# Optimization experiments

Measured on AMD Instinct MI355X. Metric: run time of the kernel, lower is better.

The kernel has to match this reference:

```python
import jax, jax.numpy as jnp
import numpy as np
import math

GAUSSIAN_KERNEL = 3.0  # sigma from init_kwargs


def setup_inputs() -> dict:
    key = jax.random.key(0)
    k1, k2, k3, k4 = jax.random.split(key, 4)
    B, De, Do, T, H, W = 4, 128, 512, 10, 32, 32
    return {
        "m_in": jax.random.normal(k1, (B, De, T, H, W), dtype=jnp.float32),
        "m_out": jax.random.normal(k2, (B, Do, T, H, W), dtype=jnp.float32),
        "q_in": jax.random.normal(k3, (B, De, H, W), dtype=jnp.float32),
        "q_out": jax.random.normal(k4, (B, Do, H, W), dtype=jnp.float32),
    }


def _gaussian_kernel_map(corr, H, W, sigma):
    # corr: [B, THW, HW]; for each memory location, gaussian centered at its
    # argmax query position over the HxW query grid.
    idx = jnp.argmax(corr, axis=2)                       # [B, THW] int
    idx_y = (idx // W).astype(corr.dtype)[..., None, None]  # [B, THW, 1, 1]
    idx_x = (idx % W).astype(corr.dtype)[..., None, None]
    y = jnp.arange(H, dtype=corr.dtype).reshape(1, 1, H, 1)
    x = jnp.arange(W, dtype=corr.dtype).reshape(1, 1, 1, W)
    g = jnp.exp(-((x - idx_x) ** 2 + (y - idx_y) ** 2) / (2.0 * sigma ** 2))
    return g.reshape(corr.shape)                         # [B, THW, HW]


def reference(m_in, m_out, q_in, q_out):
    B, De, T, H, W = m_in.shape
    Do = m_out.shape[1]
    THW, HW = T * H * W, H * W

    mi = m_in.reshape(B, De, THW)       # [B, De, THW]
    qi = q_in.reshape(B, De, HW)        # [B, De, HW]
    # p[b, t, q] = <memory key t, query key q> / sqrt(De)
    p = jnp.einsum('bdt,bdq->btq', mi, qi) / math.sqrt(De)   # [B, THW, HW]

    gauss = _gaussian_kernel_map(p, H, W, GAUSSIAN_KERNEL)

    # softmax over memory dimension (dim=1), then gaussian reweight + renorm
    p_soft = jax.nn.softmax(p, axis=1)
    p_w = p_soft * gauss
    p_w = p_w / jnp.sum(p_w, axis=1, keepdims=True)

    mo = m_out.reshape(B, Do, THW)
    mem = jnp.einsum('bdt,btq->bdq', mo, p_w).reshape(B, Do, H, W)
    mem_out = jnp.concatenate([mem, q_out], axis=1)      # [B, 2*Do, H, W]
    return mem_out, p_w
```

## Files before the change

kernel.cpp:

```cpp
#include <hip/hip_runtime.h>
#include <hip/hip_bf16.h>

#define BB 4
#define DE 128
#define DO_ 512
#define THW 10240
#define HW 1024
#define SCALE 0.08838834764831845f
#define INV2S2 0.05555555555555555f
#define NCH 32
#define CHT 320

#define WS_PART_F  81920
#define WS_STATS_F 344064
#define WS_MO16_B  1409024ull
#define WS_PWT_B   43352064ull
#define WS_MITH_B  (WS_PWT_B)
#define WS_MITL_B  (WS_PWT_B + 10485760ull)
#define WS_QITH_B  (WS_PWT_B + 20971520ull)
#define WS_QITL_B  (WS_PWT_B + 22020096ull)

using bf16x8 = __attribute__((ext_vector_type(8))) short;
using f16x8  = __attribute__((ext_vector_type(8))) _Float16;
using f32x4  = __attribute__((ext_vector_type(4))) float;
using u16x8  = __attribute__((ext_vector_type(8))) unsigned short;

__device__ __forceinline__ unsigned short f2bf(float f) {
    __hip_bfloat16 h = __float2bfloat16(f);
    return *reinterpret_cast<unsigned short*>(&h);
}
__device__ __forceinline__ void glds16(const void* g, void* l) {
    __builtin_amdgcn_global_load_lds((const __attribute__((address_space(1))) void*)g,
                                     (__attribute__((address_space(3))) void*)l,
                                     16, 0, 0);
}
__device__ __forceinline__ unsigned int ordf(float f) {
    unsigned int u = __float_as_uint(f);
    return (u & 0x80000000u) ? ~u : (u | 0x80000000u);
}

__global__ __launch_bounds__(256) void k_init(float* __restrict__ out,
                                              const float* __restrict__ qout,
                                              float4* __restrict__ amax4)
{
    int idx = blockIdx.x * 256 + threadIdx.x;
    if (idx < 20480) amax4[idx] = make_float4(0.f, 0.f, 0.f, 0.f);
    int b  = idx >> 18;
    int r  = idx & 262143;
    int c  = r >> 8;
    int q4 = r & 255;
    float4* dst = (float4*)out + idx;
    if (c < DO_) {
        *dst = make_float4(0.f, 0.f, 0.f, 0.f);
    } else {
        const float4* src = (const float4*)qout + ((size_t)(b * DO_ + (c - DO_)) << 8) + q4;
        *dst = *src;
    }
}

__global__ __launch_bounds__(256) void k_split(const float* __restrict__ src,
                                               unsigned short* __restrict__ dstH,
                                               unsigned short* __restrict__ dstL,
                                               int ncols, float scale)
{
    __shared__ float tile[128][65];
    int t0 = blockIdx.x * 64;
    int b  = blockIdx.z;
    int tid = threadIdx.x;
    const float* S = src + (size_t)b * DE * ncols + t0;
#pragma unroll
    for (int i = 0; i < 8; ++i) {
        int s  = tid + i * 256;
        int k  = s >> 4;
        int c4 = (s & 15) << 2;
        *(float4*)&tile[k][c4] = *(const float4*)&S[(size_t)k * ncols + c4];
    }
    __syncthreads();
#pragma unroll
    for (int i = 0; i < 4; ++i) {
        int s  = tid + i * 256;
        int t  = s >> 4;
        int k8 = s & 15;
        u16x8 oh, ol;
#pragma unroll
        for (int j = 0; j < 8; ++j) {
            float v = tile[k8 * 8 + j][t] * scale;
            _Float16 h = (_Float16)v;
            float rr = v - (float)h;
            _Float16 l = (_Float16)(rr * 2048.0f);
            oh[j] = *(unsigned short*)&h;
            ol[j] = *(unsigned short*)&l;
        }
        size_t o = ((size_t)b * ncols + t0 + t) * 128 + k8 * 8;
        *(u16x8*)&dstH[o] = oh;
        *(u16x8*)&dstL[o] = ol;
    }
}

__global__ __launch_bounds__(256) void k_gemm1m(const unsigned short* __restrict__ AH,
                                                const unsigned short* __restrict__ AL,
                                                const unsigned short* __restrict__ BH,
                                                const unsigned short* __restrict__ BL,
                                                float* __restrict__ p,
                                                unsigned long long* __restrict__ amax)
{
    __shared__ unsigned short AsH[4096];
    __shared__ unsigned short AsL[4096];
    __shared__ unsigned short BsH[4096];
    __shared__ unsigned short BsL[4096];
    int id  = blockIdx.x;
    int tbg = id & 7;
    int rr  = id >> 3;
    int b   = rr / 80;
    int j   = rr - b * 80;
    int tb  = tbg * 10 + (j >> 3);
    int qb  = j & 7;
    int tid = threadIdx.x;
    int w = tid >> 6, lane = tid & 63;
    int quad = lane >> 4, l15 = lane & 15;

    const char* AgH = (const char*)AH + ((size_t)b * THW + (size_t)tb * 128) * 256;
    const char* AgL = (const char*)AL + ((size_t)b * THW + (size_t)tb * 128) * 256;
    const char* BgH = (const char*)BH + ((size_t)b * HW + qb * 128) * 256;
    const char* BgL = (const char*)BL + ((size_t)b * HW + qb * 128) * 256;

    int srow = lane >> 2;
    int sj   = (lane & 3) ^ (srow & 3);
    size_t ro0 = (size_t)(w * 32 + srow) * 256 + sj * 16;
    size_t ro1 = (size_t)(w * 32 + 16 + srow) * 256 + sj * 16;
    char* lds0[4] = {(char*)AsH + w * 2048, (char*)AsL + w * 2048,
                     (char*)BsH + w * 2048, (char*)BsL + w * 2048};
    const char* gl0[4] = {AgH, AgL, BgH, BgL};

    int wm = w >> 1, wn = w & 1;
    int fq = ((l15 & 3) ^ quad) << 4;
    const char* aFH = (const char*)AsH + (wm * 64 + l15) * 64 + fq;
    const char* aFL = (const char*)AsL + (wm * 64 + l15) * 64 + fq;
    const char* bFH = (const char*)BsH + (wn * 64 + l15) * 64 + fq;
    const char* bFL = (const char*)BsL + (wn * 64 + l15) * 64 + fq;

    f32x4 acc1[4][4], acc2[4][4];
#pragma unroll
    for (int i = 0; i < 4; ++i)
#pragma unroll
        for (int j2 = 0; j2 < 4; ++j2) {
            acc1[i][j2] = (f32x4){0.f, 0.f, 0.f, 0.f};
            acc2[i][j2] = (f32x4){0.f, 0.f, 0.f, 0.f};
        }

    for (int kc = 0; kc < 4; ++kc) {
        size_t kb = (size_t)kc * 64;
        __syncthreads();
#pragma unroll
        for (int m = 0; m < 4; ++m) {
            glds16(gl0[m] + ro0 + kb, lds0[m]);
            glds16(gl0[m] + ro1 + kb, lds0[m] + 1024);
        }
        __syncthreads();
        f16x8 afH[4], afL[4], bfH[4], bfL[4];
#pragma unroll
        for (int i = 0; i < 4; ++i) {
            afH[i] = *(const f16x8*)(aFH + i * 1024);
            afL[i] = *(const f16x8*)(aFL + i * 1024);
            bfH[i] = *(const f16x8*)(bFH + i * 1024);
            bfL[i] = *(const f16x8*)(bFL + i * 1024);
        }
#pragma unroll
        for (int i = 0; i < 4; ++i)
#pragma unroll
            for (int j2 = 0; j2 < 4; ++j2)
                acc1[i][j2] = __builtin_amdgcn_mfma_f32_16x16x32_f16(afH[i], bfH[j2], acc1[i][j2], 0, 0, 0);
#pragma unroll
        for (int i = 0; i < 4; ++i)
#pragma unroll
            for (int j2 = 0; j2 < 4; ++j2)
                acc2[i][j2] = __builtin_amdgcn_mfma_f32_16x16x32_f16(afH[i], bfL[j2], acc2[i][j2], 0, 0, 0);
#pragma unroll
        for (int i = 0; i < 4; ++i)
#pragma unroll
            for (int j2 = 0; j2 < 4; ++j2)
                acc2[i][j2] = __builtin_amdgcn_mfma_f32_16x16x32_f16(afL[i], bfH[j2], acc2[i][j2], 0, 0, 0);
    }

    const float inv2048 = 4.8828125e-4f;
    int t0 = tb * 128 + wm * 64;
    float* Pg = p + ((size_t)b * THW + t0) * HW + qb * 128 + wn * 64;
    int qbase = qb * 128 + wn * 64;
#pragma unroll
    for (int i = 0; i < 4; ++i) {
#pragma unroll
        for (int r = 0; r < 4; ++r) {
            int tl = i * 16 + quad * 4 + r;
            float v[4];
#pragma unroll
            for (int j2 = 0; j2 < 4; ++j2) {
                v[j2] = acc1[i][j2][r] + acc2[i][j2][r] * inv2048;
                Pg[(size_t)tl * HW + j2 * 16 + l15] = v[j2];
            }
            float best = v[0]; int bj = 0;
#pragma unroll
            for (int j2 = 1; j2 < 4; ++j2)
                if (v[j2] > best) { best = v[j2]; bj = j2; }
            int q = qbase + bj * 16 + l15;
            unsigned long long pk = ((unsigned long long)ordf(best) << 32)
                                  | (unsigned long long)(0xFFFFFFFFu - (unsigned)q);
#pragma unroll
            for (int off = 1; off < 16; off <<= 1) {
                unsigned long long o = __shfl_xor(pk, off);
                if (o > pk) pk = o;
            }
            if (l15 == 0)
                atomicMax(&amax[(size_t)b * THW + t0 + tl], pk);
        }
    }
}

__global__ __launch_bounds__(256) void k_colstats(const float* __restrict__ p,
                                                  const unsigned long long* __restrict__ amax,
                                                  float* __restrict__ part)
{
    int q  = blockIdx.x * 256 + threadIdx.x;
    int ch = blockIdx.y, b = blockIdx.z;
    float x = (float)(q & 31), y = (float)(q >> 5);
    const float* pp = p + ((size_t)b * THW + ch * CHT) * HW + q;
    const unsigned long long* am = amax + (size_t)b * THW + ch * CHT;
    float m = -3.0e38f, s = 0.f;
    for (int i = 0; i < CHT; ++i) {
        unsigned idx = 0xFFFFFFFFu - (unsigned)am[i];
        float dx = x - (float)(idx & 31), dy = y - (float)(idx >> 5);
        float z = pp[(size_t)i * HW] - (dx * dx + dy * dy) * INV2S2;
        float nm = fmaxf(m, z);
        s = s * __expf(m - nm) + __expf(z - nm);
        m = nm;
    }
    size_t o = ((size_t)(b * NCH + ch) * HW + q) * 2;
    part[o] = m; part[o + 1] = s;
}

__global__ __launch_bounds__(256) void k_reduce(const float* __restrict__ part,
                                                float* __restrict__ stats)
{
    int i = blockIdx.x * 256 + threadIdx.x;
    int b = i >> 10, q = i & 1023;
    float M = -3.0e38f;
#pragma unroll
    for (int c = 0; c < NCH; ++c)
        M = fmaxf(M, part[((size_t)(b * NCH + c) * HW + q) * 2]);
    float S = 0.f;
#pragma unroll
    for (int c = 0; c < NCH; ++c) {
        size_t o = ((size_t)(b * NCH + c) * HW + q) * 2;
        S += part[o + 1] * __expf(part[o] - M);
    }
    stats[(size_t)i * 2] = M;
    stats[(size_t)i * 2 + 1] = 1.0f / S;
}

__global__ __launch_bounds__(256) void k_pwt(float* __restrict__ p,
                                             const unsigned long long* __restrict__ amax,
                                             const float* __restrict__ stats,
                                             unsigned short* __restrict__ pwT)
{
    __shared__ float tile[64][65];
    __shared__ float ctr[128];
    __shared__ float st[128];
    int qb = blockIdx.x, tb = blockIdx.y, b = blockIdx.z;
    int tid = threadIdx.x;
    if (tid < 64) {
        unsigned idx = 0xFFFFFFFFu - (unsigned)amax[(size_t)b * THW + tb * 64 + tid];
        ctr[tid * 2]     = (float)(idx & 31);
        ctr[tid * 2 + 1] = (float)(idx >> 5);
    }
    if (tid < 128)
        st[tid] = stats[((size_t)b * HW + qb * 64) * 2 + tid];
    __syncthreads();
    int r0 = tid >> 4;
    int c4 = (tid & 15) << 2;
#pragma unroll
    for (int i = 0; i < 4; ++i) {
        int r = r0 + i * 16;
        float* pp = p + ((size_t)b * THW + tb * 64 + r) * HW + qb * 64 + c4;
        float4 v = *(float4*)pp;
        float cx = ctr[r * 2], cy = ctr[r * 2 + 1];
        float vv[4] = {v.x, v.y, v.z, v.w};
#pragma unroll
        for (int j = 0; j < 4; ++j) {
            int q = qb * 64 + c4 + j;
            float x = (float)(q & 31), y = (float)(q >> 5);
            float dx = x - cx, dy = y - cy;
            vv[j] = __expf(vv[j] - (dx * dx + dy * dy) * INV2S2 - st[(c4 + j) * 2])
                    * st[(c4 + j) * 2 + 1];
            tile[r][c4 + j] = vv[j];
        }
        *(float4*)pp = make_float4(vv[0], vv[1], vv[2], vv[3]);
    }
    __syncthreads();
    int ql = tid >> 3;
    int t0 = (tid & 7) << 3;
#pragma unroll
    for (int pass = 0; pass < 2; ++pass) {
        int q = ql + pass * 32;
        u16x8 o8;
#pragma unroll
        for (int j = 0; j < 8; ++j)
            o8[j] = f2bf(tile[t0 + j][q]);
        *(u16x8*)&pwT[((size_t)b * HW + qb * 64 + q) * THW + tb * 64 + t0] = o8;
    }
}

__global__ __launch_bounds__(256) void k_mo16(const float* __restrict__ mo,
                                              unsigned short* __restrict__ o)
{
    size_t base = ((size_t)blockIdx.x * 256 + threadIdx.x) * 8;
    float4 a = *(const float4*)(mo + base);
    float4 c = *(const float4*)(mo + base + 4);
    u16x8 v;
    v[0] = f2bf(a.x); v[1] = f2bf(a.y); v[2] = f2bf(a.z); v[3] = f2bf(a.w);
    v[4] = f2bf(c.x); v[5] = f2bf(c.y); v[6] = f2bf(c.z); v[7] = f2bf(c.w);
    *(u16x8*)(o + base) = v;
}

__global__ __launch_bounds__(256) void k_gemm2m(const unsigned short* __restrict__ A16,
                                                const unsigned short* __restrict__ B16,
                                                float* __restrict__ out)
{
    __shared__ unsigned short As[4096];
    __shared__ unsigned short Bs[4096];
    int id   = blockIdx.x;
    int xcd  = id & 7;
    int rest = id >> 3;
    int shi  = rest >> 5;
    int jj   = rest & 31;
    int s    = xcd + (shi << 3);
    int b    = s >> 2, ks = s & 3;
    int mb   = jj >> 3, nb = jj & 7;
    int tid = threadIdx.x;
    int w = tid >> 6, lane = tid & 63;
    int quad = lane >> 4, l15 = lane & 15;

    const char* Ag = (const char*)(A16 + (size_t)b * DO_ * THW + (size_t)mb * 128 * THW + ks * 2560);
    const char* Bg = (const char*)(B16 + (size_t)b * HW * THW + (size_t)nb * 128 * THW + ks * 2560);

    int srow = lane >> 2;
    int sj   = (lane & 3) ^ (srow & 3);
    const char* aP0 = Ag + (size_t)((w * 2 + 0) * 16 + srow) * (THW * 2) + sj * 16;
    const char* aP1 = Ag + (size_t)((w * 2 + 1) * 16 + srow) * (THW * 2) + sj * 16;
    const char* bP0 = Bg + (size_t)((w * 2 + 0) * 16 + srow) * (THW * 2) + sj * 16;
    const char* bP1 = Bg + (size_t)((w * 2 + 1) * 16 + srow) * (THW * 2) + sj * 16;
    char* lA0 = (char*)As + (w * 2 + 0) * 1024;
    char* lA1 = (char*)As + (w * 2 + 1) * 1024;
    char* lB0 = (char*)Bs + (w * 2 + 0) * 1024;
    char* lB1 = (char*)Bs + (w * 2 + 1) * 1024;

    int wm = w >> 1, wn = w & 1;
    int fq = ((l15 & 3) ^ quad) << 4;
    const char* aF = (const char*)As + (wm * 64 + l15) * 64 + fq;
    const char* bF = (const char*)Bs + (wn * 64 + l15) * 64 + fq;

    f32x4 acc[4][4];
#pragma unroll
    for (int i = 0; i < 4; ++i)
#pragma unroll
        for (int j = 0; j < 4; ++j)
            acc[i][j] = (f32x4){0.f, 0.f, 0.f, 0.f};

    for (int kit = 0; kit < 80; ++kit) {
        int kb = kit * 64;
        __syncthreads();
        glds16(aP0 + kb, lA0);
        glds16(aP1 + kb, lA1);
        glds16(bP0 + kb, lB0);
        glds16(bP1 + kb, lB1);
        __syncthreads();
        bf16x8 af[4], bfr[4];
#pragma unroll
        for (int i = 0; i < 4; ++i) af[i]  = *(const bf16x8*)(aF + i * 1024);
#pragma unroll
        for (int j = 0; j < 4; ++j) bfr[j] = *(const bf16x8*)(bF + j * 1024);
#pragma unroll
        for (int i = 0; i < 4; ++i)
#pragma unroll
            for (int j = 0; j < 4; ++j)
                acc[i][j] = __builtin_amdgcn_mfma_f32_16x16x32_bf16(af[i], bfr[j], acc[i][j], 0, 0, 0);
    }

    float* Cg = out + (size_t)b * (2 * DO_ * HW);
    int d0 = mb * 128 + wm * 64 + quad * 4;
    int q0 = nb * 128 + wn * 64 + l15;
#pragma unroll
    for (int i = 0; i < 4; ++i)
#pragma unroll
        for (int j = 0; j < 4; ++j)
#pragma unroll
            for (int r = 0; r < 4; ++r)
                atomicAdd(&Cg[(size_t)(d0 + i * 16 + r) * HW + q0 + j * 16], acc[i][j][r]);
}

extern "C" void kernel_launch(void* const* d_in, const int* in_sizes, int n_in,
                              void* d_out, int out_size, void* d_ws, size_t ws_size,
                              hipStream_t stream)
{
    const float* m_in  = (const float*)d_in[0];
    const float* m_out = (const float*)d_in[1];
    const float* q_in  = (const float*)d_in[2];
    const float* q_out = (const float*)d_in[3];
    float* out = (float*)d_out;
    float* pw  = out + (size_t)BB * 2 * DO_ * HW;
    float* ws  = (float*)d_ws;
    unsigned long long* amax = (unsigned long long*)d_ws;
    float* part    = ws + WS_PART_F;
    float* stats   = ws + WS_STATS_F;
    unsigned short* mo16  = (unsigned short*)((char*)d_ws + WS_MO16_B);
    unsigned short* pwT16 = (unsigned short*)((char*)d_ws + WS_PWT_B);
    unsigned short* miTH  = (unsigned short*)((char*)d_ws + WS_MITH_B);
    unsigned short* miTL  = (unsigned short*)((char*)d_ws + WS_MITL_B);
    unsigned short* qiTH  = (unsigned short*)((char*)d_ws + WS_QITH_B);
    unsigned short* qiTL  = (unsigned short*)((char*)d_ws + WS_QITL_B);

    hipLaunchKernelGGL(k_init,    dim3(4096),        dim3(256), 0, stream, out, q_out, (float4*)d_ws);
    hipLaunchKernelGGL(k_split,   dim3(160, 1, BB),  dim3(256), 0, stream, m_in, miTH, miTL, THW, 1.0f);
    hipLaunchKernelGGL(k_split,   dim3(16, 1, BB),   dim3(256), 0, stream, q_in, qiTH, qiTL, HW, SCALE);
    hipLaunchKernelGGL(k_gemm1m,  dim3(2560),        dim3(256), 0, stream, miTH, miTL, qiTH, qiTL, pw, amax);
    hipLaunchKernelGGL(k_colstats,dim3(4, NCH, BB),  dim3(256), 0, stream, pw, amax, part);
    hipLaunchKernelGGL(k_reduce,  dim3(16),          dim3(256), 0, stream, part, stats);
    hipLaunchKernelGGL(k_mo16,    dim3(10240),       dim3(256), 0, stream, m_out, mo16);
    hipLaunchKernelGGL(k_pwt,     dim3(16, 160, BB), dim3(256), 0, stream, pw, amax, stats, pwT16);
    hipLaunchKernelGGL(k_gemm2m,  dim3(512),         dim3(256), 0, stream, mo16, pwT16, out);
}
```

Measured before the change: 516.8 us.

## Double-buffer LDS staging in both GEMMs and double split-K in gemm2

Both MFMA GEMM kernels now use two LDS buffers, issuing global-to-LDS loads for the next K chunk before computing on the current one, with explicit vmcnt waits and raw barriers replacing the two syncthreads per iteration. The second GEMM also splits K eight ways instead of four, doubling the grid to 1024 blocks with half the K iterations each. The aim is to hide global load latency and raise occupancy and parallelism on the output GEMM. The cost is doubled shared memory per block, which may reduce resident blocks, and twice as many atomic adds into the output.

```diff
diff --git a/kernel.cpp b/kernel.cpp
--- a/kernel.cpp
+++ b/kernel.cpp
@@ -104,10 +104,10 @@
                                                 float* __restrict__ p,
                                                 unsigned long long* __restrict__ amax)
 {
-    __shared__ unsigned short AsH[4096];
-    __shared__ unsigned short AsL[4096];
-    __shared__ unsigned short BsH[4096];
-    __shared__ unsigned short BsL[4096];
+    __shared__ unsigned short AsH[2][4096];
+    __shared__ unsigned short AsL[2][4096];
+    __shared__ unsigned short BsH[2][4096];
+    __shared__ unsigned short BsL[2][4096];
     int id  = blockIdx.x;
     int tbg = id & 7;
     int rr  = id >> 3;
@@ -128,9 +128,18 @@
     int sj   = (lane & 3) ^ (srow & 3);
     size_t ro0 = (size_t)(w * 32 + srow) * 256 + sj * 16;
     size_t ro1 = (size_t)(w * 32 + 16 + srow) * 256 + sj * 16;
-    char* lds0[4] = {(char*)AsH + w * 2048, (char*)AsL + w * 2048,
-                     (char*)BsH + w * 2048, (char*)BsL + w * 2048};
-    const char* gl0[4] = {AgH, AgL, BgH, BgL};
+
+#define G1_STAGE(BUF, KB) do {                                                          \
+    char* _d;                                                                           \
+    _d = (char*)AsH + (BUF) * 8192 + w * 2048;                                          \
+    glds16(AgH + ro0 + (KB), _d); glds16(AgH + ro1 + (KB), _d + 1024);                  \
+    _d = (char*)AsL + (BUF) * 8192 + w * 2048;                                          \
+    glds16(AgL + ro0 + (KB), _d); glds16(AgL + ro1 + (KB), _d + 1024);                  \
+    _d = (char*)BsH + (BUF) * 8192 + w * 2048;                                          \
+    glds16(BgH + ro0 + (KB), _d); glds16(BgH + ro1 + (KB), _d + 1024);                  \
+    _d = (char*)BsL + (BUF) * 8192 + w * 2048;                                          \
+    glds16(BgL + ro0 + (KB), _d); glds16(BgL + ro1 + (KB), _d + 1024);                  \
+  } while (0)
 
     int wm = w >> 1, wn = w & 1;
     int fq = ((l15 & 3) ^ quad) << 4;
@@ -148,22 +157,25 @@
             acc2[i][j2] = (f32x4){0.f, 0.f, 0.f, 0.f};
         }
 
+    G1_STAGE(0, 0);
+    int cur = 0;
     for (int kc = 0; kc < 4; ++kc) {
-        size_t kb = (size_t)kc * 64;
-        __syncthreads();
-#pragma unroll
-        for (int m = 0; m < 4; ++m) {
-            glds16(gl0[m] + ro0 + kb, lds0[m]);
-            glds16(gl0[m] + ro1 + kb, lds0[m] + 1024);
-        }
-        __syncthreads();
+        if (kc < 3) {
+            G1_STAGE(cur ^ 1, (size_t)(kc + 1) * 64);
+            asm volatile("s_waitcnt vmcnt(8)" ::: "memory");
+        } else {
+            asm volatile("s_waitcnt vmcnt(0)" ::: "memory");
+        }
+        __builtin_amdgcn_s_barrier();
+        __builtin_amdgcn_sched_barrier(0);
+        int cb = cur * 8192;
         f16x8 afH[4], afL[4], bfH[4], bfL[4];
 #pragma unroll
         for (int i = 0; i < 4; ++i) {
-            afH[i] = *(const f16x8*)(aFH + i * 1024);
-            afL[i] = *(const f16x8*)(aFL + i * 1024);
-            bfH[i] = *(const f16x8*)(bFH + i * 1024);
-            bfL[i] = *(const f16x8*)(bFL + i * 1024);
+            afH[i] = *(const f16x8*)(aFH + cb + i * 1024);
+            afL[i] = *(const f16x8*)(aFL + cb + i * 1024);
+            bfH[i] = *(const f16x8*)(bFH + cb + i * 1024);
+            bfL[i] = *(const f16x8*)(bFL + cb + i * 1024);
         }
 #pragma unroll
         for (int i = 0; i < 4; ++i)
@@ -180,7 +192,11 @@
 #pragma unroll
             for (int j2 = 0; j2 < 4; ++j2)
                 acc2[i][j2] = __builtin_amdgcn_mfma_f32_16x16x32_f16(afL[i], bfH[j2], acc2[i][j2], 0, 0, 0);
-    }
+        __builtin_amdgcn_sched_barrier(0);
+        __builtin_amdgcn_s_barrier();
+        cur ^= 1;
+    }
+#undef G1_STAGE
 
     const float inv2048 = 4.8828125e-4f;
     int t0 = tb * 128 + wm * 64;
@@ -324,22 +340,22 @@
                                                 const unsigned short* __restrict__ B16,
                                                 float* __restrict__ out)
 {
-    __shared__ unsigned short As[4096];
-    __shared__ unsigned short Bs[4096];
+    __shared__ unsigned short As[2][4096];
+    __shared__ unsigned short Bs[2][4096];
     int id   = blockIdx.x;
     int xcd  = id & 7;
     int rest = id >> 3;
     int shi  = rest >> 5;
     int jj   = rest & 31;
     int s    = xcd + (shi << 3);
-    int b    = s >> 2, ks = s & 3;
+    int b    = s >> 3, ks = s & 7;
     int mb   = jj >> 3, nb = jj & 7;
     int tid = threadIdx.x;
     int w = tid >> 6, lane = tid & 63;
     int quad = lane >> 4, l15 = lane & 15;
 
-    const char* Ag = (const char*)(A16 + (size_t)b * DO_ * THW + (size_t)mb * 128 * THW + ks * 2560);
-    const char* Bg = (const char*)(B16 + (size_t)b * HW * THW + (size_t)nb * 128 * THW + ks * 2560);
+    const char* Ag = (const char*)(A16 + (size_t)b * DO_ * THW + (size_t)mb * 128 * THW + ks * 1280);
+    const char* Bg = (const char*)(B16 + (size_t)b * HW * THW + (size_t)nb * 128 * THW + ks * 1280);
 
     int srow = lane >> 2;
     int sj   = (lane & 3) ^ (srow & 3);
@@ -352,6 +368,13 @@
     char* lB0 = (char*)Bs + (w * 2 + 0) * 1024;
     char* lB1 = (char*)Bs + (w * 2 + 1) * 1024;
 
+#define G2_STAGE(BUF, KB) do {                          \
+    glds16(aP0 + (KB), lA0 + (BUF) * 8192);             \
+    glds16(aP1 + (KB), lA1 + (BUF) * 8192);             \
+    glds16(bP0 + (KB), lB0 + (BUF) * 8192);             \
+    glds16(bP1 + (KB), lB1 + (BUF) * 8192);             \
+  } while (0)
+
     int wm = w >> 1, wn = w & 1;
     int fq = ((l15 & 3) ^ quad) << 4;
     const char* aF = (const char*)As + (wm * 64 + l15) * 64 + fq;
@@ -364,25 +387,33 @@
         for (int j = 0; j < 4; ++j)
             acc[i][j] = (f32x4){0.f, 0.f, 0.f, 0.f};
 
-    for (int kit = 0; kit < 80; ++kit) {
-        int kb = kit * 64;
-        __syncthreads();
-        glds16(aP0 + kb, lA0);
-        glds16(aP1 + kb, lA1);
-        glds16(bP0 + kb, lB0);
-        glds16(bP1 + kb, lB1);
-        __syncthreads();
+    G2_STAGE(0, 0);
+    int cur = 0;
+    for (int kit = 0; kit < 40; ++kit) {
+        if (kit < 39) {
+            G2_STAGE(cur ^ 1, (size_t)(kit + 1) * 64);
+            asm volatile("s_waitcnt vmcnt(4)" ::: "memory");
+        } else {
+            asm volatile("s_waitcnt vmcnt(0)" ::: "memory");
+        }
+        __builtin_amdgcn_s_barrier();
+        __builtin_amdgcn_sched_barrier(0);
+        int cb = cur * 8192;
         bf16x8 af[4], bfr[4];
 #pragma unroll
-        for (int i = 0; i < 4; ++i) af[i]  = *(const bf16x8*)(aF + i * 1024);
-#pragma unroll
-        for (int j = 0; j < 4; ++j) bfr[j] = *(const bf16x8*)(bF + j * 1024);
+        for (int i = 0; i < 4; ++i) af[i]  = *(const bf16x8*)(aF + cb + i * 1024);
+#pragma unroll
+        for (int j = 0; j < 4; ++j) bfr[j] = *(const bf16x8*)(bF + cb + j * 1024);
 #pragma unroll
         for (int i = 0; i < 4; ++i)
 #pragma unroll
             for (int j = 0; j < 4; ++j)
                 acc[i][j] = __builtin_amdgcn_mfma_f32_16x16x32_bf16(af[i], bfr[j], acc[i][j], 0, 0, 0);
-    }
+        __builtin_amdgcn_sched_barrier(0);
+        __builtin_amdgcn_s_barrier();
+        cur ^= 1;
+    }
+#undef G2_STAGE
 
     float* Cg = out + (size_t)b * (2 * DO_ * HW);
     int d0 = mb * 128 + wm * 64 + quad * 4;
@@ -425,5 +456,5 @@
     hipLaunchKernelGGL(k_reduce,  dim3(16),          dim3(256), 0, stream, part, stats);
     hipLaunchKernelGGL(k_mo16,    dim3(10240),       dim3(256), 0, stream, m_out, mo16);
     hipLaunchKernelGGL(k_pwt,     dim3(16, 160, BB), dim3(256), 0, stream, pw, amax, stats, pwT16);
-    hipLaunchKernelGGL(k_gemm2m,  dim3(512),         dim3(256), 0, stream, mo16, pwT16, out);
-}
+    hipLaunchKernelGGL(k_gemm2m,  dim3(1024),        dim3(256), 0, stream, mo16, pwT16, out);
+}
```

New measurement: 517.8 us. Within noise of the previous version (+0.2%).

## Load GEMM fragments directly from global and drop split-K atomics in second GEMM

Applied to the files above, without the earlier changes.

Both MFMA GEMMs stop staging tiles through LDS and instead load f16/bf16 fragments straight from global memory into registers. The first GEMM drops its barriers and LDS buffers. The second GEMM drops the 4-way split-K with atomicAdd in favour of full-K blocks with a 128x64 tile, 256 blocks, register double-buffering and plain stores. This removes LDS barriers and atomic traffic on the output, at the cost of losing shared-memory reuse across waves and adding more strided global loads per wave.

```diff
diff --git a/kernel.cpp b/kernel.cpp
--- a/kernel.cpp
+++ b/kernel.cpp
@@ -28,11 +28,6 @@
 __device__ __forceinline__ unsigned short f2bf(float f) {
     __hip_bfloat16 h = __float2bfloat16(f);
     return *reinterpret_cast<unsigned short*>(&h);
-}
-__device__ __forceinline__ void glds16(const void* g, void* l) {
-    __builtin_amdgcn_global_load_lds((const __attribute__((address_space(1))) void*)g,
-                                     (__attribute__((address_space(3))) void*)l,
-                                     16, 0, 0);
 }
 __device__ __forceinline__ unsigned int ordf(float f) {
     unsigned int u = __float_as_uint(f);
@@ -97,17 +92,13 @@
     }
 }
 
-__global__ __launch_bounds__(256) void k_gemm1m(const unsigned short* __restrict__ AH,
+__global__ __launch_bounds__(256) void k_gemm1r(const unsigned short* __restrict__ AH,
                                                 const unsigned short* __restrict__ AL,
                                                 const unsigned short* __restrict__ BH,
                                                 const unsigned short* __restrict__ BL,
                                                 float* __restrict__ p,
                                                 unsigned long long* __restrict__ amax)
 {
-    __shared__ unsigned short AsH[4096];
-    __shared__ unsigned short AsL[4096];
-    __shared__ unsigned short BsH[4096];
-    __shared__ unsigned short BsL[4096];
     int id  = blockIdx.x;
     int tbg = id & 7;
     int rr  = id >> 3;
@@ -118,26 +109,14 @@
     int tid = threadIdx.x;
     int w = tid >> 6, lane = tid & 63;
     int quad = lane >> 4, l15 = lane & 15;
-
-    const char* AgH = (const char*)AH + ((size_t)b * THW + (size_t)tb * 128) * 256;
-    const char* AgL = (const char*)AL + ((size_t)b * THW + (size_t)tb * 128) * 256;
-    const char* BgH = (const char*)BH + ((size_t)b * HW + qb * 128) * 256;
-    const char* BgL = (const char*)BL + ((size_t)b * HW + qb * 128) * 256;
-
-    int srow = lane >> 2;
-    int sj   = (lane & 3) ^ (srow & 3);
-    size_t ro0 = (size_t)(w * 32 + srow) * 256 + sj * 16;
-    size_t ro1 = (size_t)(w * 32 + 16 + srow) * 256 + sj * 16;
-    char* lds0[4] = {(char*)AsH + w * 2048, (char*)AsL + w * 2048,
-                     (char*)BsH + w * 2048, (char*)BsL + w * 2048};
-    const char* gl0[4] = {AgH, AgL, BgH, BgL};
-
     int wm = w >> 1, wn = w & 1;
-    int fq = ((l15 & 3) ^ quad) << 4;
-    const char* aFH = (const char*)AsH + (wm * 64 + l15) * 64 + fq;
-    const char* aFL = (const char*)AsL + (wm * 64 + l15) * 64 + fq;
-    const char* bFH = (const char*)BsH + (wn * 64 + l15) * 64 + fq;
-    const char* bFL = (const char*)BsL + (wn * 64 + l15) * 64 + fq;
+
+    size_t aoff = ((size_t)b * THW + (size_t)tb * 128 + wm * 64 + l15) * 128 + quad * 8;
+    size_t boff = ((size_t)b * HW + qb * 128 + wn * 64 + l15) * 128 + quad * 8;
+    const unsigned short* aHp = AH + aoff;
+    const unsigned short* aLp = AL + aoff;
+    const unsigned short* bHp = BH + boff;
+    const unsigned short* bLp = BL + boff;
 
     f32x4 acc1[4][4], acc2[4][4];
 #pragma unroll
@@ -148,22 +127,15 @@
             acc2[i][j2] = (f32x4){0.f, 0.f, 0.f, 0.f};
         }
 
+#pragma unroll
     for (int kc = 0; kc < 4; ++kc) {
-        size_t kb = (size_t)kc * 64;
-        __syncthreads();
-#pragma unroll
-        for (int m = 0; m < 4; ++m) {
-            glds16(gl0[m] + ro0 + kb, lds0[m]);
-            glds16(gl0[m] + ro1 + kb, lds0[m] + 1024);
-        }
-        __syncthreads();
         f16x8 afH[4], afL[4], bfH[4], bfL[4];
 #pragma unroll
         for (int i = 0; i < 4; ++i) {
-            afH[i] = *(const f16x8*)(aFH + i * 1024);
-            afL[i] = *(const f16x8*)(aFL + i * 1024);
-            bfH[i] = *(const f16x8*)(bFH + i * 1024);
-            bfL[i] = *(const f16x8*)(bFL + i * 1024);
+            afH[i] = *(const f16x8*)(aHp + i * 2048 + kc * 32);
+            afL[i] = *(const f16x8*)(aLp + i * 2048 + kc * 32);
+            bfH[i] = *(const f16x8*)(bHp + i * 2048 + kc * 32);
+            bfL[i] = *(const f16x8*)(bLp + i * 2048 + kc * 32);
         }
 #pragma unroll
         for (int i = 0; i < 4; ++i)
@@ -320,80 +292,85 @@
     *(u16x8*)(o + base) = v;
 }
 
-__global__ __launch_bounds__(256) void k_gemm2m(const unsigned short* __restrict__ A16,
+__global__ __launch_bounds__(256) void k_gemm2r(const unsigned short* __restrict__ A16,
                                                 const unsigned short* __restrict__ B16,
                                                 float* __restrict__ out)
 {
-    __shared__ unsigned short As[4096];
-    __shared__ unsigned short Bs[4096];
-    int id   = blockIdx.x;
-    int xcd  = id & 7;
-    int rest = id >> 3;
-    int shi  = rest >> 5;
-    int jj   = rest & 31;
-    int s    = xcd + (shi << 3);
-    int b    = s >> 2, ks = s & 3;
-    int mb   = jj >> 3, nb = jj & 7;
+    int id  = blockIdx.x;
+    int xcd = id & 7;
+    int j   = id >> 3;
+    int pair = xcd * 2 + (j >> 4);
+    int b  = pair >> 2, mb = pair & 3;
+    int nb = j & 15;
     int tid = threadIdx.x;
     int w = tid >> 6, lane = tid & 63;
     int quad = lane >> 4, l15 = lane & 15;
-
-    const char* Ag = (const char*)(A16 + (size_t)b * DO_ * THW + (size_t)mb * 128 * THW + ks * 2560);
-    const char* Bg = (const char*)(B16 + (size_t)b * HW * THW + (size_t)nb * 128 * THW + ks * 2560);
-
-    int srow = lane >> 2;
-    int sj   = (lane & 3) ^ (srow & 3);
-    const char* aP0 = Ag + (size_t)((w * 2 + 0) * 16 + srow) * (THW * 2) + sj * 16;
-    const char* aP1 = Ag + (size_t)((w * 2 + 1) * 16 + srow) * (THW * 2) + sj * 16;
-    const char* bP0 = Bg + (size_t)((w * 2 + 0) * 16 + srow) * (THW * 2) + sj * 16;
-    const char* bP1 = Bg + (size_t)((w * 2 + 1) * 16 + srow) * (THW * 2) + sj * 16;
-    char* lA0 = (char*)As + (w * 2 + 0) * 1024;
-    char* lA1 = (char*)As + (w * 2 + 1) * 1024;
-    char* lB0 = (char*)Bs + (w * 2 + 0) * 1024;
-    char* lB1 = (char*)Bs + (w * 2 + 1) * 1024;
-
     int wm = w >> 1, wn = w & 1;
-    int fq = ((l15 & 3) ^ quad) << 4;
-    const char* aF = (const char*)As + (wm * 64 + l15) * 64 + fq;
-    const char* bF = (const char*)Bs + (wn * 64 + l15) * 64 + fq;
-
-    f32x4 acc[4][4];
+
+    const unsigned short* aB[4];
+    const unsigned short* bB[2];
 #pragma unroll
     for (int i = 0; i < 4; ++i)
-#pragma unroll
-        for (int j = 0; j < 4; ++j)
-            acc[i][j] = (f32x4){0.f, 0.f, 0.f, 0.f};
-
-    for (int kit = 0; kit < 80; ++kit) {
-        int kb = kit * 64;
-        __syncthreads();
-        glds16(aP0 + kb, lA0);
-        glds16(aP1 + kb, lA1);
-        glds16(bP0 + kb, lB0);
-        glds16(bP1 + kb, lB1);
-        __syncthreads();
-        bf16x8 af[4], bfr[4];
-#pragma unroll
-        for (int i = 0; i < 4; ++i) af[i]  = *(const bf16x8*)(aF + i * 1024);
-#pragma unroll
-        for (int j = 0; j < 4; ++j) bfr[j] = *(const bf16x8*)(bF + j * 1024);
-#pragma unroll
-        for (int i = 0; i < 4; ++i)
-#pragma unroll
-            for (int j = 0; j < 4; ++j)
-                acc[i][j] = __builtin_amdgcn_mfma_f32_16x16x32_bf16(af[i], bfr[j], acc[i][j], 0, 0, 0);
-    }
+        aB[i] = A16 + ((size_t)b * DO_ + mb * 128 + wm * 64 + i * 16 + l15) * THW + quad * 8;
+#pragma unroll
+    for (int jj = 0; jj < 2; ++jj)
+        bB[jj] = B16 + ((size_t)b * HW + nb * 64 + wn * 32 + jj * 16 + l15) * THW + quad * 8;
+
+#define G2_LOAD(AS, BS, KIT) do {                                              \
+    _Pragma("unroll")                                                          \
+    for (int i = 0; i < 4; ++i) {                                              \
+        AS[i]     = *(const bf16x8*)(aB[i] + (size_t)(KIT) * 64);              \
+        AS[i + 4] = *(const bf16x8*)(aB[i] + (size_t)(KIT) * 64 + 32);         \
+    }                                                                          \
+    _Pragma("unroll")                                                          \
+    for (int jj = 0; jj < 2; ++jj) {                                           \
+        BS[jj]     = *(const bf16x8*)(bB[jj] + (size_t)(KIT) * 64);            \
+        BS[jj + 2] = *(const bf16x8*)(bB[jj] + (size_t)(KIT) * 64 + 32);       \
+    }                                                                          \
+  } while (0)
+
+#define G2_MFMA(AS, BS) do {                                                   \
+    _Pragma("unroll")                                                          \
+    for (int i = 0; i < 4; ++i)                                                \
+        _Pragma("unroll")                                                      \
+        for (int jj = 0; jj < 2; ++jj)                                         \
+            acc[i][jj] = __builtin_amdgcn_mfma_f32_16x16x32_bf16(AS[i], BS[jj], acc[i][jj], 0, 0, 0); \
+    _Pragma("unroll")                                                          \
+    for (int i = 0; i < 4; ++i)                                                \
+        _Pragma("unroll")                                                      \
+        for (int jj = 0; jj < 2; ++jj)                                         \
+            acc[i][jj] = __builtin_amdgcn_mfma_f32_16x16x32_bf16(AS[i + 4], BS[jj + 2], acc[i][jj], 0, 0, 0); \
+  } while (0)
+
+    f32x4 acc[4][2];
+#pragma unroll
+    for (int i = 0; i < 4; ++i)
+#pragma unroll
+        for (int jj = 0; jj < 2; ++jj)
+            acc[i][jj] = (f32x4){0.f, 0.f, 0.f, 0.f};
+
+    bf16x8 a0[8], a1[8], b0[4], b1[4];
+    G2_LOAD(a0, b0, 0);
+    for (int kit = 0; kit < 160; kit += 2) {
+        G2_LOAD(a1, b1, kit + 1);
+        G2_MFMA(a0, b0);
+        if (kit < 158)
+            G2_LOAD(a0, b0, kit + 2);
+        G2_MFMA(a1, b1);
+    }
+#undef G2_LOAD
+#undef G2_MFMA
 
     float* Cg = out + (size_t)b * (2 * DO_ * HW);
     int d0 = mb * 128 + wm * 64 + quad * 4;
-    int q0 = nb * 128 + wn * 64 + l15;
+    int q0 = nb * 64 + wn * 32 + l15;
 #pragma unroll
     for (int i = 0; i < 4; ++i)
 #pragma unroll
-        for (int j = 0; j < 4; ++j)
+        for (int jj = 0; jj < 2; ++jj)
 #pragma unroll
             for (int r = 0; r < 4; ++r)
-                atomicAdd(&Cg[(size_t)(d0 + i * 16 + r) * HW + q0 + j * 16], acc[i][j][r]);
+                Cg[(size_t)(d0 + i * 16 + r) * HW + q0 + jj * 16] = acc[i][jj][r];
 }
 
 extern "C" void kernel_launch(void* const* d_in, const int* in_sizes, int n_in,
@@ -420,10 +397,10 @@
     hipLaunchKernelGGL(k_init,    dim3(4096),        dim3(256), 0, stream, out, q_out, (float4*)d_ws);
     hipLaunchKernelGGL(k_split,   dim3(160, 1, BB),  dim3(256), 0, stream, m_in, miTH, miTL, THW, 1.0f);
     hipLaunchKernelGGL(k_split,   dim3(16, 1, BB),   dim3(256), 0, stream, q_in, qiTH, qiTL, HW, SCALE);
-    hipLaunchKernelGGL(k_gemm1m,  dim3(2560),        dim3(256), 0, stream, miTH, miTL, qiTH, qiTL, pw, amax);
+    hipLaunchKernelGGL(k_gemm1r,  dim3(2560),        dim3(256), 0, stream, miTH, miTL, qiTH, qiTL, pw, amax);
     hipLaunchKernelGGL(k_colstats,dim3(4, NCH, BB),  dim3(256), 0, stream, pw, amax, part);
     hipLaunchKernelGGL(k_reduce,  dim3(16),          dim3(256), 0, stream, part, stats);
     hipLaunchKernelGGL(k_mo16,    dim3(10240),       dim3(256), 0, stream, m_out, mo16);
     hipLaunchKernelGGL(k_pwt,     dim3(16, 160, BB), dim3(256), 0, stream, pw, amax, stats, pwT16);
-    hipLaunchKernelGGL(k_gemm2m,  dim3(512),         dim3(256), 0, stream, mo16, pwT16, out);
-}
+    hipLaunchKernelGGL(k_gemm2r,  dim3(256),         dim3(256), 0, stream, mo16, pwT16, out);
+}
```

New measurement: 695.2 us. 1.35x slower.
